# Performance work log

Measured on AMD Instinct MI355X. Metric: run time of the kernel, lower is better.

## Reference

```python
import jax, jax.numpy as jnp
import numpy as np

B, T, D, F, E, TOP_K = 4, 1024, 1024, 4096, 8, 2


def setup_inputs() -> dict:
    key = jax.random.key(0)
    k0, k1, k2, k3, k4 = jax.random.split(key, 5)
    x = jax.random.normal(k0, (B, T, D), dtype=jnp.float32)
    # xavier-uniform-ish scales
    Wr = jax.random.normal(k1, (D, E), dtype=jnp.float32) * (1.0 / np.sqrt(D))
    W1 = jax.random.normal(k2, (E, D, F), dtype=jnp.float32) * (1.0 / np.sqrt(D))
    W3 = jax.random.normal(k3, (E, D, F), dtype=jnp.float32) * (1.0 / np.sqrt(D))
    W2 = jax.random.normal(k4, (E, F, D), dtype=jnp.float32) * (1.0 / np.sqrt(F))
    return {"x": x, "Wr": Wr, "W1": W1, "W3": W3, "W2": W2}


def reference(x, Wr, W1, W3, W2):
    # Router: logits [B,T,E]
    logits = jnp.einsum('btd,de->bte', x, Wr)
    top_vals, top_idx = jax.lax.top_k(logits, TOP_K)          # [B,T,K]
    weights = jax.nn.softmax(top_vals, axis=-1)               # [B,T,K]
    probs = jax.nn.softmax(logits, axis=-1)                   # [B,T,E]
    usage = probs.mean(axis=(0, 1))                           # [E]
    load_balancing_loss = E * jnp.sum(usage ** 2)

    # SwiGLU experts computed densely per expert: down(silu(gate(x)) * up(x))
    gate = jnp.einsum('btd,edf->ebtf', x, W1)                 # [E,B,T,F]
    up = jnp.einsum('btd,edf->ebtf', x, W3)
    h = jax.nn.silu(gate) * up
    eout = jnp.einsum('ebtf,efd->ebtd', h, W2)                # [E,B,T,D]
    eout = jnp.moveaxis(eout, 0, 2)                           # [B,T,E,D]

    # Gather selected experts and combine with softmax weights
    sel = jnp.take_along_axis(eout, top_idx[..., None], axis=2)  # [B,T,K,D]
    output = jnp.sum(sel * weights[..., None], axis=2)           # [B,T,D]
    return output, load_balancing_loss
```

## Files before the change

kernel.cpp:

```cpp
#include <hip/hip_runtime.h>
#include <hip/hip_bf16.h>
#include <stdint.h>
#include <math.h>

#define NTOK 4096
#define DDIM 1024
#define FDIM 4096
#define NEXP 8
#define NPAIR 8192

#define BM 256
#define BN 64
#define BK 64

#define RT_TPW 8
#define RT_BLOCKS (NTOK / (4 * RT_TPW))

using short8 = __attribute__((ext_vector_type(8))) short;
using f32x4  = __attribute__((ext_vector_type(4))) float;

__device__ __forceinline__ uint16_t f2bf(float f) {
    union { float f; uint32_t u; } v; v.f = f;
    uint32_t r = v.u + 0x7FFFu + ((v.u >> 16) & 1u);
    return (uint16_t)(r >> 16);
}

__device__ __forceinline__ void async16(const void* g, void* l) {
    __builtin_amdgcn_global_load_lds((const __attribute__((address_space(1))) void*)g,
                                     (__attribute__((address_space(3))) void*)l,
                                     16, 0, 0);
}

__global__ void router_kernel(const float* __restrict__ x, const float* __restrict__ Wr,
                              int* __restrict__ cnt_part, float* __restrict__ us_part,
                              int* __restrict__ top_e, float* __restrict__ top_w) {
    __shared__ float us[NEXP];
    __shared__ int cs[NEXP];
    const int tid = threadIdx.x;
    const int wv = tid >> 6;
    const int lane = tid & 63;
    if (tid < NEXP) { us[tid] = 0.f; cs[tid] = 0; }
    __syncthreads();

    for (int i = 0; i < RT_TPW; i++) {
        const int t = blockIdx.x * (4 * RT_TPW) + wv * RT_TPW + i;
        float acc[NEXP];
#pragma unroll
        for (int e = 0; e < NEXP; e++) acc[e] = 0.f;
        const float* xr = x + (size_t)t * DDIM;
        for (int d = lane; d < DDIM; d += 64) {
            float xv = xr[d];
            const float* wr = Wr + (size_t)d * NEXP;
#pragma unroll
            for (int e = 0; e < NEXP; e++) acc[e] += xv * wr[e];
        }
#pragma unroll
        for (int e = 0; e < NEXP; e++) {
#pragma unroll
            for (int off = 32; off > 0; off >>= 1) acc[e] += __shfl_xor(acc[e], off, 64);
        }
        if (lane == 0) {
            int i0 = 0;
#pragma unroll
            for (int e = 1; e < NEXP; e++) if (acc[e] > acc[i0]) i0 = e;
            int i1 = -1;
#pragma unroll
            for (int e = 0; e < NEXP; e++) {
                if (e == i0) continue;
                if (i1 < 0 || acc[e] > acc[i1]) i1 = e;
            }
            float v0 = acc[i0], v1 = acc[i1];
            float e1 = __expf(v1 - v0);
            float inv = 1.f / (1.f + e1);
            top_e[t * 2 + 0] = i0; top_e[t * 2 + 1] = i1;
            top_w[t * 2 + 0] = inv; top_w[t * 2 + 1] = e1 * inv;
            atomicAdd(&cs[i0], 1);
            atomicAdd(&cs[i1], 1);
            float m = acc[0];
#pragma unroll
            for (int e = 1; e < NEXP; e++) m = fmaxf(m, acc[e]);
            float p[NEXP]; float s = 0.f;
#pragma unroll
            for (int e = 0; e < NEXP; e++) { p[e] = __expf(acc[e] - m); s += p[e]; }
            float is = 1.f / s;
#pragma unroll
            for (int e = 0; e < NEXP; e++) atomicAdd(&us[e], p[e] * is);
        }
    }
    __syncthreads();
    if (tid < NEXP) {
        cnt_part[blockIdx.x * NEXP + tid] = cs[tid];
        us_part[blockIdx.x * NEXP + tid] = us[tid];
    }
}

__global__ void finalize_kernel(const int* __restrict__ cnt_part, const float* __restrict__ us_part,
                                int* __restrict__ counts, int* __restrict__ offs,
                                float* __restrict__ out) {
    __shared__ int c[NEXP];
    __shared__ float u[NEXP];
    const int tid = threadIdx.x;
    if (tid < NEXP) {
        int csum = 0; float usum = 0.f;
        for (int b = 0; b < RT_BLOCKS; b++) {
            csum += cnt_part[b * NEXP + tid];
            usum += us_part[b * NEXP + tid];
        }
        counts[tid] = csum; c[tid] = csum; u[tid] = usum;
    }
    __syncthreads();
    if (tid == 0) {
        int s = 0; float l = 0.f;
#pragma unroll
        for (int e = 0; e < NEXP; e++) {
            offs[e] = s; s += c[e];
            float uu = u[e] * (1.f / (float)NTOK);
            l += uu * uu;
        }
        out[(size_t)NTOK * DDIM] = (float)NEXP * l;
    }
}

__global__ void xcast_kernel(const float* __restrict__ x, uint16_t* __restrict__ xb) {
    int i = blockIdx.x * 256 + threadIdx.x;
    float4 v = ((const float4*)x)[i];
    ushort4 o;
    o.x = f2bf(v.x); o.y = f2bf(v.y); o.z = f2bf(v.z); o.w = f2bf(v.w);
    ((ushort4*)xb)[i] = o;
}

__global__ void transpose_cast_kernel(const float* __restrict__ in, uint16_t* __restrict__ outp,
                                      int R, int C) {
    __shared__ uint16_t tile[64 * 64];
    const int e = blockIdx.z;
    const float* src = in + (size_t)e * R * C;
    uint16_t* dst = outp + (size_t)e * R * C;
    const int r0 = blockIdx.y * 64, c0 = blockIdx.x * 64;
    const int t = threadIdx.x;
    {
        const int rb = t >> 4;
        const int c4 = t & 15;
#pragma unroll
        for (int i = 0; i < 4; i++) {
            const int r = rb + i * 16;
            float4 v = *(const float4*)(src + (size_t)(r0 + r) * C + c0 + c4 * 4);
            const int rc = (r >> 3);
            const int re = (r & 7);
#pragma unroll
            for (int j = 0; j < 4; j++) {
                const int c = c4 * 4 + j;
                float fv = (j == 0) ? v.x : (j == 1) ? v.y : (j == 2) ? v.z : v.w;
                tile[c * 64 + ((rc ^ (c & 7)) << 3) + re] = f2bf(fv);
            }
        }
    }
    __syncthreads();
    {
        const int cr = t >> 3;
        const int ch = t & 7;
#pragma unroll
        for (int i = 0; i < 2; i++) {
            const int c = cr + i * 32;
            uint4 v = *(const uint4*)&tile[c * 64 + ((ch ^ (c & 7)) << 3)];
            *(uint4*)(dst + (size_t)(c0 + c) * R + r0 + ch * 8) = v;
        }
    }
}

__global__ void scatter_kernel(const int* __restrict__ top_e, const float* __restrict__ top_w,
                               const int* __restrict__ offs, int* __restrict__ fill,
                               int* __restrict__ pair_tok, float* __restrict__ pair_w) {
    __shared__ int lcnt[NEXP];
    __shared__ int lbase[NEXP];
    const int tid = threadIdx.x;
    const int t = blockIdx.x * 256 + tid;
    if (tid < NEXP) lcnt[tid] = 0;
    __syncthreads();
    int e0 = top_e[t * 2 + 0], e1 = top_e[t * 2 + 1];
    int r0 = atomicAdd(&lcnt[e0], 1);
    int r1 = atomicAdd(&lcnt[e1], 1);
    __syncthreads();
    if (tid < NEXP) lbase[tid] = atomicAdd(&fill[tid], lcnt[tid]);
    __syncthreads();
    int p0 = offs[e0] + lbase[e0] + r0;
    int p1 = offs[e1] + lbase[e1] + r1;
    pair_tok[p0] = t; pair_w[p0] = top_w[t * 2 + 0];
    pair_tok[p1] = t; pair_w[p1] = top_w[t * 2 + 1];
}

__global__ __launch_bounds__(256, 2)
void expert_up_kernel(const uint16_t* __restrict__ x_bf,
                      const uint16_t* __restrict__ W1t, const uint16_t* __restrict__ W3t,
                      const int* __restrict__ counts, const int* __restrict__ offs,
                      const int* __restrict__ pair_tok, uint16_t* __restrict__ h) {
    const int e = blockIdx.z;
    const int tile = blockIdx.y;
    const int n0 = blockIdx.x * BN;
    const int cntAll = counts[e];
    if (tile * BM >= cntAll) return;
    const int cnt = min(BM, cntAll - tile * BM);
    const int pairBase = offs[e] + tile * BM;

    __shared__ uint16_t As[BM * BK];
    __shared__ uint16_t B1s[BN * BK];
    __shared__ uint16_t B3s[BN * BK];

    const int tid = threadIdx.x;
    const int wave = tid >> 6;
    const int lane = tid & 63;
    const int quad = lane >> 4;
    const int lr = lane & 15;
    const int sub = lane >> 3;
    const int swoff = (((lane & 7) ^ sub) << 3);

    int tokr[8];
#pragma unroll
    for (int i = 0; i < 8; i++) {
        int row = wave * 64 + i * 8 + sub;
        tokr[i] = pair_tok[pairBase + min(row, cnt - 1)];
    }
    const uint16_t* w1p = W1t + (size_t)e * DDIM * FDIM;
    const uint16_t* w3p = W3t + (size_t)e * DDIM * FDIM;

    f32x4 accG[4][4], accU[4][4];
#pragma unroll
    for (int i = 0; i < 4; i++)
#pragma unroll
        for (int j = 0; j < 4; j++) {
            accG[i][j] = (f32x4){0.f, 0.f, 0.f, 0.f};
            accU[i][j] = (f32x4){0.f, 0.f, 0.f, 0.f};
        }

    for (int k0 = 0; k0 < DDIM; k0 += BK) {
        __syncthreads();
#pragma unroll
        for (int i = 0; i < 8; i++)
            async16(x_bf + (size_t)tokr[i] * DDIM + k0 + swoff,
                    &As[(wave * 64 + i * 8) * BK] + lane * 8);
#pragma unroll
        for (int j = 0; j < 2; j++) {
            int n = wave * 16 + j * 8 + sub;
            async16(w1p + (size_t)(n0 + n) * DDIM + k0 + swoff,
                    &B1s[(wave * 16 + j * 8) * BK] + lane * 8);
            async16(w3p + (size_t)(n0 + n) * DDIM + k0 + swoff,
                    &B3s[(wave * 16 + j * 8) * BK] + lane * 8);
        }
        __syncthreads();
#pragma unroll
        for (int kk = 0; kk < BK; kk += 32) {
            const int lc = (kk >> 3) + quad;
            short8 af[4];
#pragma unroll
            for (int mi = 0; mi < 4; mi++) {
                int R = wave * 64 + mi * 16 + lr;
                af[mi] = *(const short8*)&As[R * BK + ((lc ^ (lr & 7)) << 3)];
            }
#pragma unroll
            for (int ni = 0; ni < 4; ni++) {
                int n = ni * 16 + lr;
                short8 b1 = *(const short8*)&B1s[n * BK + ((lc ^ (lr & 7)) << 3)];
                short8 b3 = *(const short8*)&B3s[n * BK + ((lc ^ (lr & 7)) << 3)];
#pragma unroll
                for (int mi = 0; mi < 4; mi++) {
                    accG[mi][ni] = __builtin_amdgcn_mfma_f32_16x16x32_bf16(af[mi], b1, accG[mi][ni], 0, 0, 0);
                    accU[mi][ni] = __builtin_amdgcn_mfma_f32_16x16x32_bf16(af[mi], b3, accU[mi][ni], 0, 0, 0);
                }
            }
        }
    }
#pragma unroll
    for (int mi = 0; mi < 4; mi++) {
#pragma unroll
        for (int r = 0; r < 4; r++) {
            int rowLocal = wave * 64 + mi * 16 + quad * 4 + r;
            if (rowLocal < cnt) {
                uint16_t* dst = h + (size_t)(pairBase + rowLocal) * FDIM + n0 + lr;
#pragma unroll
                for (int ni = 0; ni < 4; ni++) {
                    float g = accG[mi][ni][r];
                    float u = accU[mi][ni][r];
                    float hv = (g / (1.f + __expf(-g))) * u;
                    dst[ni * 16] = f2bf(hv);
                }
            }
        }
    }
}

__global__ __launch_bounds__(256, 3)
void expert_down_kernel(const uint16_t* __restrict__ h, const uint16_t* __restrict__ W2t,
                        const int* __restrict__ counts, const int* __restrict__ offs,
                        const int* __restrict__ pair_tok, const float* __restrict__ pair_w,
                        float* __restrict__ out) {
    const int e = blockIdx.z;
    const int tile = blockIdx.y;
    const int n0 = blockIdx.x * BN;
    const int cntAll = counts[e];
    if (tile * BM >= cntAll) return;
    const int cnt = min(BM, cntAll - tile * BM);
    const int pairBase = offs[e] + tile * BM;

    __shared__ uint16_t As[BM * BK];
    __shared__ uint16_t Bs[BN * BK];

    const int tid = threadIdx.x;
    const int wave = tid >> 6;
    const int lane = tid & 63;
    const int quad = lane >> 4;
    const int lr = lane & 15;
    const int sub = lane >> 3;
    const int swoff = (((lane & 7) ^ sub) << 3);

    int hrow[8];
#pragma unroll
    for (int i = 0; i < 8; i++) {
        int row = wave * 64 + i * 8 + sub;
        hrow[i] = pairBase + min(row, cnt - 1);
    }
    const uint16_t* w2p = W2t + (size_t)e * FDIM * DDIM;

    f32x4 acc[4][4];
#pragma unroll
    for (int i = 0; i < 4; i++)
#pragma unroll
        for (int j = 0; j < 4; j++) acc[i][j] = (f32x4){0.f, 0.f, 0.f, 0.f};

    for (int k0 = 0; k0 < FDIM; k0 += BK) {
        __syncthreads();
#pragma unroll
        for (int i = 0; i < 8; i++)
            async16(h + (size_t)hrow[i] * FDIM + k0 + swoff,
                    &As[(wave * 64 + i * 8) * BK] + lane * 8);
#pragma unroll
        for (int j = 0; j < 2; j++) {
            int n = wave * 16 + j * 8 + sub;
            async16(w2p + (size_t)(n0 + n) * FDIM + k0 + swoff,
                    &Bs[(wave * 16 + j * 8) * BK] + lane * 8);
        }
        __syncthreads();
#pragma unroll
        for (int kk = 0; kk < BK; kk += 32) {
            const int lc = (kk >> 3) + quad;
            short8 af[4];
#pragma unroll
            for (int mi = 0; mi < 4; mi++) {
                int R = wave * 64 + mi * 16 + lr;
                af[mi] = *(const short8*)&As[R * BK + ((lc ^ (lr & 7)) << 3)];
            }
#pragma unroll
            for (int ni = 0; ni < 4; ni++) {
                int n = ni * 16 + lr;
                short8 b = *(const short8*)&Bs[n * BK + ((lc ^ (lr & 7)) << 3)];
#pragma unroll
                for (int mi = 0; mi < 4; mi++)
                    acc[mi][ni] = __builtin_amdgcn_mfma_f32_16x16x32_bf16(af[mi], b, acc[mi][ni], 0, 0, 0);
            }
        }
    }
#pragma unroll
    for (int mi = 0; mi < 4; mi++) {
#pragma unroll
        for (int r = 0; r < 4; r++) {
            int rowLocal = wave * 64 + mi * 16 + quad * 4 + r;
            if (rowLocal < cnt) {
                int pi = pairBase + rowLocal;
                int tok = pair_tok[pi];
                float w = pair_w[pi];
                float* dst = out + (size_t)tok * DDIM + n0 + lr;
#pragma unroll
                for (int ni = 0; ni < 4; ni++)
                    atomicAdd(&dst[ni * 16], acc[mi][ni][r] * w);
            }
        }
    }
}

extern "C" void kernel_launch(void* const* d_in, const int* in_sizes, int n_in,
                              void* d_out, int out_size, void* d_ws, size_t ws_size,
                              hipStream_t stream) {
    (void)in_sizes; (void)n_in; (void)ws_size;
    const float* x  = (const float*)d_in[0];
    const float* Wr = (const float*)d_in[1];
    const float* W1 = (const float*)d_in[2];
    const float* W3 = (const float*)d_in[3];
    const float* W2 = (const float*)d_in[4];
    float* out = (float*)d_out;

    char* ws = (char*)d_ws;
    size_t off = 0;
    int*      counts    = (int*)(ws + off);  off += 64;
    int*      offs      = (int*)(ws + off);  off += 64;
    int*      fill      = (int*)(ws + off);  off += 128;
    int*      top_e     = (int*)(ws + off);  off += 4 * NPAIR;
    float*    top_w     = (float*)(ws + off); off += 4 * NPAIR;
    int*      pair_tok  = (int*)(ws + off);  off += 4 * NPAIR;
    float*    pair_w    = (float*)(ws + off); off += 4 * NPAIR;
    int*      cnt_part  = (int*)(ws + off);  off += 4 * RT_BLOCKS * NEXP;
    float*    us_part   = (float*)(ws + off); off += 4 * RT_BLOCKS * NEXP;
    uint16_t* x_bf      = (uint16_t*)(ws + off); off += (size_t)2 * NTOK * DDIM;
    uint16_t* h         = (uint16_t*)(ws + off); off += (size_t)2 * NPAIR * FDIM;
    const size_t wBytes = (size_t)2 * NEXP * DDIM * FDIM;
    uint16_t* W1t = (uint16_t*)(ws + off);
    uint16_t* W3t = (uint16_t*)(ws + off + wBytes);
    uint16_t* W2t = (uint16_t*)(ws + off + 2 * wBytes);

    hipMemsetAsync(ws, 0, 256, stream);
    hipMemsetAsync(d_out, 0, (size_t)out_size * sizeof(float), stream);

    xcast_kernel<<<NTOK * DDIM / 1024, 256, 0, stream>>>(x, x_bf);
    router_kernel<<<RT_BLOCKS, 256, 0, stream>>>(x, Wr, cnt_part, us_part, top_e, top_w);
    finalize_kernel<<<1, 64, 0, stream>>>(cnt_part, us_part, counts, offs, out);
    scatter_kernel<<<NTOK / 256, 256, 0, stream>>>(top_e, top_w, offs, fill, pair_tok, pair_w);

    transpose_cast_kernel<<<dim3(FDIM / 64, DDIM / 64, NEXP), 256, 0, stream>>>(W1, W1t, DDIM, FDIM);
    transpose_cast_kernel<<<dim3(FDIM / 64, DDIM / 64, NEXP), 256, 0, stream>>>(W3, W3t, DDIM, FDIM);
    transpose_cast_kernel<<<dim3(DDIM / 64, FDIM / 64, NEXP), 256, 0, stream>>>(W2, W2t, FDIM, DDIM);

    dim3 gA(FDIM / BN, NTOK / BM, NEXP);
    expert_up_kernel<<<gA, 256, 0, stream>>>(x_bf, W1t, W3t, counts, offs, pair_tok, h);
    dim3 gB(DDIM / BN, NTOK / BM, NEXP);
    expert_down_kernel<<<gB, 256, 0, stream>>>(h, W2t, counts, offs, pair_tok, pair_w, out);
}
```

Baseline: 813.4 us.

## Interleave W1/W3 weights and pipeline up-projection GEMM with 4-stage async buffers

The W1 and W3 transposes now write into one interleaved buffer, alternating 16-column groups of gate and up, so the up-projection GEMM treats gate and up as a single 256-wide N tile. The up kernel is rewritten for 512 threads with a 256x256 output tile, BK=32, a 4-deep async shared-memory ring with explicit vmcnt waits, barriers and setprio around the MFMA bursts. The goal is better data reuse per block and overlap of global loads with MFMA work. In exchange it uses large shared memory (128KB) and many accumulator registers, which may limit occupancy.

```diff
diff --git a/kernel.cpp b/kernel.cpp
--- a/kernel.cpp
+++ b/kernel.cpp
@@ -130,11 +130,12 @@
 }
 
 __global__ void transpose_cast_kernel(const float* __restrict__ in, uint16_t* __restrict__ outp,
-                                      int R, int C) {
+                                      int R, int C, int sel) {
     __shared__ uint16_t tile[64 * 64];
     const int e = blockIdx.z;
     const float* src = in + (size_t)e * R * C;
-    uint16_t* dst = outp + (size_t)e * R * C;
+    const size_t osz = (size_t)R * C * (sel < 0 ? 1 : 2);
+    uint16_t* dst = outp + (size_t)e * osz;
     const int r0 = blockIdx.y * 64, c0 = blockIdx.x * 64;
     const int t = threadIdx.x;
     {
@@ -162,7 +163,9 @@
         for (int i = 0; i < 2; i++) {
             const int c = cr + i * 32;
             uint4 v = *(const uint4*)&tile[c * 64 + ((ch ^ (c & 7)) << 3)];
-            *(uint4*)(dst + (size_t)(c0 + c) * R + r0 + ch * 8) = v;
+            const int oc = c0 + c;
+            const int orow = (sel < 0) ? oc : (((oc >> 4) << 5) + sel + (oc & 15));
+            *(uint4*)(dst + (size_t)orow * R + r0 + ch * 8) = v;
         }
     }
 }
@@ -188,99 +191,107 @@
     pair_tok[p1] = t; pair_w[p1] = top_w[t * 2 + 1];
 }
 
-__global__ __launch_bounds__(256, 2)
+__global__ __launch_bounds__(512, 2)
 void expert_up_kernel(const uint16_t* __restrict__ x_bf,
-                      const uint16_t* __restrict__ W1t, const uint16_t* __restrict__ W3t,
+                      const uint16_t* __restrict__ W13t,
                       const int* __restrict__ counts, const int* __restrict__ offs,
                       const int* __restrict__ pair_tok, uint16_t* __restrict__ h) {
     const int e = blockIdx.z;
     const int tile = blockIdx.y;
-    const int n0 = blockIdx.x * BN;
     const int cntAll = counts[e];
-    if (tile * BM >= cntAll) return;
-    const int cnt = min(BM, cntAll - tile * BM);
-    const int pairBase = offs[e] + tile * BM;
-
-    __shared__ uint16_t As[BM * BK];
-    __shared__ uint16_t B1s[BN * BK];
-    __shared__ uint16_t B3s[BN * BK];
+    if (tile * 256 >= cntAll) return;
+    const int cnt = min(256, cntAll - tile * 256);
+    const int pairBase = offs[e] + tile * 256;
+    const int bx = blockIdx.x;
+
+    __shared__ uint16_t smem[4 * 16384];
 
     const int tid = threadIdx.x;
-    const int wave = tid >> 6;
-    const int lane = tid & 63;
-    const int quad = lane >> 4;
-    const int lr = lane & 15;
-    const int sub = lane >> 3;
-    const int swoff = (((lane & 7) ^ sub) << 3);
-
-    int tokr[8];
-#pragma unroll
-    for (int i = 0; i < 8; i++) {
-        int row = wave * 64 + i * 8 + sub;
-        tokr[i] = pair_tok[pairBase + min(row, cnt - 1)];
-    }
-    const uint16_t* w1p = W1t + (size_t)e * DDIM * FDIM;
-    const uint16_t* w3p = W3t + (size_t)e * DDIM * FDIM;
-
-    f32x4 accG[4][4], accU[4][4];
-#pragma unroll
-    for (int i = 0; i < 4; i++)
-#pragma unroll
-        for (int j = 0; j < 4; j++) {
-            accG[i][j] = (f32x4){0.f, 0.f, 0.f, 0.f};
-            accU[i][j] = (f32x4){0.f, 0.f, 0.f, 0.f};
-        }
-
-    for (int k0 = 0; k0 < DDIM; k0 += BK) {
-        __syncthreads();
-#pragma unroll
-        for (int i = 0; i < 8; i++)
-            async16(x_bf + (size_t)tokr[i] * DDIM + k0 + swoff,
-                    &As[(wave * 64 + i * 8) * BK] + lane * 8);
-#pragma unroll
-        for (int j = 0; j < 2; j++) {
-            int n = wave * 16 + j * 8 + sub;
-            async16(w1p + (size_t)(n0 + n) * DDIM + k0 + swoff,
-                    &B1s[(wave * 16 + j * 8) * BK] + lane * 8);
-            async16(w3p + (size_t)(n0 + n) * DDIM + k0 + swoff,
-                    &B3s[(wave * 16 + j * 8) * BK] + lane * 8);
-        }
-        __syncthreads();
-#pragma unroll
-        for (int kk = 0; kk < BK; kk += 32) {
-            const int lc = (kk >> 3) + quad;
-            short8 af[4];
-#pragma unroll
-            for (int mi = 0; mi < 4; mi++) {
-                int R = wave * 64 + mi * 16 + lr;
-                af[mi] = *(const short8*)&As[R * BK + ((lc ^ (lr & 7)) << 3)];
-            }
-#pragma unroll
-            for (int ni = 0; ni < 4; ni++) {
-                int n = ni * 16 + lr;
-                short8 b1 = *(const short8*)&B1s[n * BK + ((lc ^ (lr & 7)) << 3)];
-                short8 b3 = *(const short8*)&B3s[n * BK + ((lc ^ (lr & 7)) << 3)];
-#pragma unroll
-                for (int mi = 0; mi < 4; mi++) {
-                    accG[mi][ni] = __builtin_amdgcn_mfma_f32_16x16x32_bf16(af[mi], b1, accG[mi][ni], 0, 0, 0);
-                    accU[mi][ni] = __builtin_amdgcn_mfma_f32_16x16x32_bf16(af[mi], b3, accU[mi][ni], 0, 0, 0);
-                }
-            }
-        }
-    }
-#pragma unroll
-    for (int mi = 0; mi < 4; mi++) {
+    const int w = tid >> 6, lane = tid & 63;
+    const int wr = w >> 2, wc = w & 3;
+    const int lr = lane & 15, q = lane >> 4;
+    const int qa = q ^ ((lr >> 1) & 3);
+    const int aoff = (wr * 128 + lr) * 32 + qa * 8;
+    const int boff = (wc * 64 + lr) * 32 + qa * 8;
+    const int q_src = (tid & 3) ^ ((tid >> 3) & 3);
+    const int ldst = tid * 8;
+
+    const int tok0 = pair_tok[pairBase + min(tid >> 2, cnt - 1)];
+    const int tok1 = pair_tok[pairBase + min(128 + (tid >> 2), cnt - 1)];
+    const uint16_t* asrc0 = x_bf + (size_t)tok0 * DDIM + q_src * 8;
+    const uint16_t* asrc1 = x_bf + (size_t)tok1 * DDIM + q_src * 8;
+    const uint16_t* bsrc = W13t + (size_t)e * 2 * FDIM * DDIM
+                         + (size_t)(bx * 256 + (tid >> 2)) * DDIM + q_src * 8;
+
+#define UP_STAGE_A(kt_) do { const int sb = ((kt_) & 3) * 16384; \
+    async16(asrc0 + (kt_) * 32, &smem[sb + ldst]); \
+    async16(asrc1 + (kt_) * 32, &smem[sb + 4096 + ldst]); } while (0)
+#define UP_STAGE_B(kt_) do { const int sb = ((kt_) & 3) * 16384 + 8192; \
+    async16(bsrc + (kt_) * 32, &smem[sb + ldst]); \
+    async16(bsrc + 131072 + (kt_) * 32, &smem[sb + 4096 + ldst]); } while (0)
+
+    f32x4 acc[8][4];
+#pragma unroll
+    for (int i = 0; i < 8; i++)
+#pragma unroll
+        for (int j = 0; j < 4; j++) acc[i][j] = (f32x4){0.f, 0.f, 0.f, 0.f};
+
+    UP_STAGE_A(0); UP_STAGE_B(0);
+    UP_STAGE_A(1); UP_STAGE_B(1);
+    UP_STAGE_A(2); UP_STAGE_B(2);
+    asm volatile("s_waitcnt vmcnt(8)" ::: "memory");
+    __builtin_amdgcn_s_barrier();
+
+    for (int kt = 0; kt < 32; ++kt) {
+        const uint16_t* A = &smem[(kt & 3) * 16384];
+        const uint16_t* B = A + 8192;
+        short8 bf[4], af[4];
+#pragma unroll
+        for (int ni = 0; ni < 4; ni++) bf[ni] = *(const short8*)(B + boff + ni * 512);
+#pragma unroll
+        for (int mi = 0; mi < 4; mi++) af[mi] = *(const short8*)(A + aoff + mi * 512);
+        if (kt < 29) UP_STAGE_A(kt + 3);
+        __builtin_amdgcn_s_barrier();
+        __builtin_amdgcn_s_setprio(1);
+#pragma unroll
+        for (int ni = 0; ni < 4; ni++)
+#pragma unroll
+            for (int mi = 0; mi < 4; mi++)
+                acc[mi][ni] = __builtin_amdgcn_mfma_f32_16x16x32_bf16(af[mi], bf[ni], acc[mi][ni], 0, 0, 0);
+        __builtin_amdgcn_s_setprio(0);
+        __builtin_amdgcn_s_barrier();
+#pragma unroll
+        for (int mi = 0; mi < 4; mi++) af[mi] = *(const short8*)(A + aoff + (mi + 4) * 512);
+        if (kt < 29) UP_STAGE_B(kt + 3);
+        __builtin_amdgcn_s_barrier();
+        __builtin_amdgcn_s_setprio(1);
+#pragma unroll
+        for (int ni = 0; ni < 4; ni++)
+#pragma unroll
+            for (int mi = 0; mi < 4; mi++)
+                acc[mi + 4][ni] = __builtin_amdgcn_mfma_f32_16x16x32_bf16(af[mi], bf[ni], acc[mi + 4][ni], 0, 0, 0);
+        __builtin_amdgcn_s_setprio(0);
+        if (kt < 29)       asm volatile("s_waitcnt vmcnt(8)" ::: "memory");
+        else if (kt == 29) asm volatile("s_waitcnt vmcnt(4)" ::: "memory");
+        else               asm volatile("s_waitcnt vmcnt(0)" ::: "memory");
+        __builtin_amdgcn_s_barrier();
+    }
+#undef UP_STAGE_A
+#undef UP_STAGE_B
+
+#pragma unroll
+    for (int mi = 0; mi < 8; mi++) {
 #pragma unroll
         for (int r = 0; r < 4; r++) {
-            int rowLocal = wave * 64 + mi * 16 + quad * 4 + r;
+            const int rowLocal = wr * 128 + mi * 16 + q * 4 + r;
             if (rowLocal < cnt) {
-                uint16_t* dst = h + (size_t)(pairBase + rowLocal) * FDIM + n0 + lr;
-#pragma unroll
-                for (int ni = 0; ni < 4; ni++) {
-                    float g = accG[mi][ni][r];
-                    float u = accU[mi][ni][r];
+                uint16_t* dst = h + (size_t)(pairBase + rowLocal) * FDIM + bx * 128 + lr;
+#pragma unroll
+                for (int j = 0; j < 2; j++) {
+                    float g = acc[mi][2 * j][r];
+                    float u = acc[mi][2 * j + 1][r];
                     float hv = (g / (1.f + __expf(-g))) * u;
-                    dst[ni * 16] = f2bf(hv);
+                    dst[(wc * 2 + j) * 16] = f2bf(hv);
                 }
             }
         }
@@ -400,9 +411,8 @@
     uint16_t* x_bf      = (uint16_t*)(ws + off); off += (size_t)2 * NTOK * DDIM;
     uint16_t* h         = (uint16_t*)(ws + off); off += (size_t)2 * NPAIR * FDIM;
     const size_t wBytes = (size_t)2 * NEXP * DDIM * FDIM;
-    uint16_t* W1t = (uint16_t*)(ws + off);
-    uint16_t* W3t = (uint16_t*)(ws + off + wBytes);
-    uint16_t* W2t = (uint16_t*)(ws + off + 2 * wBytes);
+    uint16_t* W13t = (uint16_t*)(ws + off);
+    uint16_t* W2t  = (uint16_t*)(ws + off + 2 * wBytes);
 
     hipMemsetAsync(ws, 0, 256, stream);
     hipMemsetAsync(d_out, 0, (size_t)out_size * sizeof(float), stream);
@@ -412,12 +422,12 @@
     finalize_kernel<<<1, 64, 0, stream>>>(cnt_part, us_part, counts, offs, out);
     scatter_kernel<<<NTOK / 256, 256, 0, stream>>>(top_e, top_w, offs, fill, pair_tok, pair_w);
 
-    transpose_cast_kernel<<<dim3(FDIM / 64, DDIM / 64, NEXP), 256, 0, stream>>>(W1, W1t, DDIM, FDIM);
-    transpose_cast_kernel<<<dim3(FDIM / 64, DDIM / 64, NEXP), 256, 0, stream>>>(W3, W3t, DDIM, FDIM);
-    transpose_cast_kernel<<<dim3(DDIM / 64, FDIM / 64, NEXP), 256, 0, stream>>>(W2, W2t, FDIM, DDIM);
-
-    dim3 gA(FDIM / BN, NTOK / BM, NEXP);
-    expert_up_kernel<<<gA, 256, 0, stream>>>(x_bf, W1t, W3t, counts, offs, pair_tok, h);
+    transpose_cast_kernel<<<dim3(FDIM / 64, DDIM / 64, NEXP), 256, 0, stream>>>(W1, W13t, DDIM, FDIM, 0);
+    transpose_cast_kernel<<<dim3(FDIM / 64, DDIM / 64, NEXP), 256, 0, stream>>>(W3, W13t, DDIM, FDIM, 16);
+    transpose_cast_kernel<<<dim3(DDIM / 64, FDIM / 64, NEXP), 256, 0, stream>>>(W2, W2t, FDIM, DDIM, -1);
+
+    dim3 gA(2 * FDIM / 256, NTOK / 256, NEXP);
+    expert_up_kernel<<<gA, 512, 0, stream>>>(x_bf, W13t, counts, offs, pair_tok, h);
     dim3 gB(DDIM / BN, NTOK / BM, NEXP);
     expert_down_kernel<<<gB, 256, 0, stream>>>(h, W2t, counts, offs, pair_tok, pair_w, out);
 }
```

After: 825.8 us. About the same (+1.5%).
